# Optimization experiments

Measured on AMD Instinct MI355X. Metric: run time of the kernel, lower is better.

## Reference

```python
import jax, jax.numpy as jnp
import numpy as np

D_MODEL = 1024
N_HEADS = 16
HEAD_DIM = D_MODEL // N_HEADS


def setup_inputs() -> dict:
    key = jax.random.key(0)
    ks = jax.random.split(key, 5)
    B, S = 4, 2048
    scale = 1.0 / np.sqrt(D_MODEL)
    return {
        "x": jax.random.normal(ks[0], (B, S, D_MODEL), dtype=jnp.float32),
        "W_q": jax.random.normal(ks[1], (D_MODEL, D_MODEL), dtype=jnp.float32) * scale,
        "W_k": jax.random.normal(ks[2], (D_MODEL, D_MODEL), dtype=jnp.float32) * scale,
        "W_v": jax.random.normal(ks[3], (D_MODEL, D_MODEL), dtype=jnp.float32) * scale,
        "W_o": jax.random.normal(ks[4], (D_MODEL, D_MODEL), dtype=jnp.float32) * scale,
    }


def reference(x, W_q, W_k, W_v, W_o):
    B, S, _ = x.shape
    # nn.Linear(d,d,bias=False): y = x @ W.T ; W stored as (out,in)
    def proj(W):
        y = jnp.einsum('bsd,ed->bse', x, W)
        return y.reshape(B, S, N_HEADS, HEAD_DIM).transpose(0, 2, 1, 3)  # (B,H,S,Dh)
    q, k, v = proj(W_q), proj(W_k), proj(W_v)
    scores = jnp.einsum('bhqd,bhkd->bhqk', q, k) / np.sqrt(HEAD_DIM)
    causal = jnp.tril(jnp.ones((S, S), dtype=bool))  # (S,S)
    scores = jnp.where(causal[None, None], scores, -jnp.inf)
    attn = jax.nn.softmax(scores, axis=-1)
    heads = jnp.einsum('bhqk,bhkd->bhqd', attn, v)
    concat = heads.transpose(0, 2, 1, 3).reshape(B, S, D_MODEL)
    return jnp.einsum('bsd,ed->bse', concat, W_o)
```

## Files before the change

kernel.cpp:

```cpp
#include <hip/hip_runtime.h>
#include <hip/hip_bf16.h>

#define D_MODEL 1024
#define N_HEADS 16
#define HEAD_DIM 64
#define BATCH 4
#define SEQ 2048
#define M_ROWS (BATCH * SEQ)

typedef __attribute__((ext_vector_type(8))) __bf16 bf16x8;
typedef __attribute__((ext_vector_type(8))) short short8;
typedef __attribute__((ext_vector_type(4))) float f32x4;

static __device__ __forceinline__ unsigned short f2bf_rne(float f) {
  unsigned int u = __float_as_uint(f);
  u += 0x7FFFu + ((u >> 16) & 1u);
  return (unsigned short)(u >> 16);
}

static __device__ __forceinline__ void gl_lds16(const unsigned short* g, unsigned short* l) {
  __builtin_amdgcn_global_load_lds((const __attribute__((address_space(1))) unsigned int*)g,
                                   (__attribute__((address_space(3))) unsigned int*)l, 16, 0, 0);
}

__global__ __launch_bounds__(256) void cvt_all(const float* __restrict__ x,
                                               const float* __restrict__ wq,
                                               const float* __restrict__ wk,
                                               const float* __restrict__ wv,
                                               const float* __restrict__ wo,
                                               unsigned short* __restrict__ xb,
                                               unsigned short* __restrict__ wqb,
                                               unsigned short* __restrict__ wkb,
                                               unsigned short* __restrict__ wvb,
                                               unsigned short* __restrict__ wob) {
  const int bid = blockIdx.x;
  const float* src;
  unsigned short* dst;
  int i;
  if (bid < 8192) {
    src = x; dst = xb; i = bid * 256 + threadIdx.x;
  } else {
    int r = bid - 8192;
    int w = r >> 10;
    i = (r & 1023) * 256 + threadIdx.x;
    switch (w) {
      case 0: src = wq; dst = wqb; break;
      case 1: src = wk; dst = wkb; break;
      case 2: src = wv; dst = wvb; break;
      default: src = wo; dst = wob; break;
    }
  }
  float4 f = reinterpret_cast<const float4*>(src)[i];
  ushort4 o;
  o.x = f2bf_rne(f.x); o.y = f2bf_rne(f.y); o.z = f2bf_rne(f.z); o.w = f2bf_rne(f.w);
  reinterpret_cast<ushort4*>(dst)[i] = o;
}

__global__ __launch_bounds__(256) void qkv_gemm(const unsigned short* __restrict__ A,
                                                const unsigned short* __restrict__ Wq,
                                                const unsigned short* __restrict__ Wk,
                                                const unsigned short* __restrict__ Wv,
                                                unsigned short* __restrict__ Qo,
                                                unsigned short* __restrict__ Ko,
                                                unsigned short* __restrict__ Vo) {
  __shared__ __align__(16) unsigned short As[128 * 32];
  __shared__ __align__(16) unsigned short Bs[128 * 32];
  const int t = threadIdx.x;
  const int widx = blockIdx.x >> 3;
  const int bn = blockIdx.x & 7, bm = blockIdx.y;
  const unsigned short* Bw = (widx == 0) ? Wq : (widx == 1) ? Wk : Wv;
  unsigned short* Cp = (widx == 0) ? Qo : (widx == 1) ? Ko : Vo;
  const float oscale = (widx == 0) ? 0.125f : 1.0f;
  const int K = D_MODEL, N = D_MODEL;

  const int wave = t >> 6, lane = t & 63;
  const int wm = (wave >> 1) * 64, wn = (wave & 1) * 64;
  const int lr = lane & 15, quad = lane >> 4;

  f32x4 acc[4][4] = {};

  for (int k0 = 0; k0 < K; k0 += 32) {
    __syncthreads();
#pragma unroll
    for (int i = 0; i < 2; i++) {
      int g = wave * 128 + i * 64 + lane;
      int row = g >> 2, col8 = (g & 3) << 3;
      gl_lds16(A + (size_t)(bm * 128 + row) * K + k0 + col8, &As[g * 8]);
      gl_lds16(Bw + (size_t)(bn * 128 + row) * K + k0 + col8, &Bs[g * 8]);
    }
    __syncthreads();

    bf16x8 af[4], bfr[4];
#pragma unroll
    for (int mt = 0; mt < 4; mt++)
      af[mt] = __builtin_bit_cast(
          bf16x8, *reinterpret_cast<const short8*>(&As[(wm + mt * 16 + lr) * 32 + quad * 8]));
#pragma unroll
    for (int nt = 0; nt < 4; nt++)
      bfr[nt] = __builtin_bit_cast(
          bf16x8, *reinterpret_cast<const short8*>(&Bs[(wn + nt * 16 + lr) * 32 + quad * 8]));
#pragma unroll
    for (int mt = 0; mt < 4; mt++)
#pragma unroll
      for (int nt = 0; nt < 4; nt++)
        acc[mt][nt] = __builtin_amdgcn_mfma_f32_16x16x32_bf16(af[mt], bfr[nt], acc[mt][nt], 0, 0, 0);
  }

#pragma unroll
  for (int mt = 0; mt < 4; mt++) {
#pragma unroll
    for (int nt = 0; nt < 4; nt++) {
      int col = bn * 128 + wn + nt * 16 + lr;
#pragma unroll
      for (int r = 0; r < 4; r++) {
        int row = bm * 128 + wm + mt * 16 + quad * 4 + r;
        Cp[(size_t)row * N + col] = f2bf_rne(acc[mt][nt][r] * oscale);
      }
    }
  }
}

__global__ __launch_bounds__(256) void gemm_bt_f32(const unsigned short* __restrict__ A,
                                                   const unsigned short* __restrict__ Bw,
                                                   float* __restrict__ Cp,
                                                   int M, int N, int K) {
  __shared__ __align__(16) unsigned short As[128 * 32];
  __shared__ __align__(16) unsigned short Bs[128 * 32];
  const int t = threadIdx.x;
  const int bn = blockIdx.x, bm = blockIdx.y;
  const int wave = t >> 6, lane = t & 63;
  const int wm = (wave >> 1) * 64, wn = (wave & 1) * 64;
  const int lr = lane & 15, quad = lane >> 4;

  f32x4 acc[4][4] = {};

  for (int k0 = 0; k0 < K; k0 += 32) {
    __syncthreads();
#pragma unroll
    for (int i = 0; i < 2; i++) {
      int g = wave * 128 + i * 64 + lane;
      int row = g >> 2, col8 = (g & 3) << 3;
      gl_lds16(A + (size_t)(bm * 128 + row) * K + k0 + col8, &As[g * 8]);
      gl_lds16(Bw + (size_t)(bn * 128 + row) * K + k0 + col8, &Bs[g * 8]);
    }
    __syncthreads();

    bf16x8 af[4], bfr[4];
#pragma unroll
    for (int mt = 0; mt < 4; mt++)
      af[mt] = __builtin_bit_cast(
          bf16x8, *reinterpret_cast<const short8*>(&As[(wm + mt * 16 + lr) * 32 + quad * 8]));
#pragma unroll
    for (int nt = 0; nt < 4; nt++)
      bfr[nt] = __builtin_bit_cast(
          bf16x8, *reinterpret_cast<const short8*>(&Bs[(wn + nt * 16 + lr) * 32 + quad * 8]));
#pragma unroll
    for (int mt = 0; mt < 4; mt++)
#pragma unroll
      for (int nt = 0; nt < 4; nt++)
        acc[mt][nt] = __builtin_amdgcn_mfma_f32_16x16x32_bf16(af[mt], bfr[nt], acc[mt][nt], 0, 0, 0);
  }

#pragma unroll
  for (int mt = 0; mt < 4; mt++) {
#pragma unroll
    for (int nt = 0; nt < 4; nt++) {
      int col = bn * 128 + wn + nt * 16 + lr;
#pragma unroll
      for (int r = 0; r < 4; r++) {
        int row = bm * 128 + wm + mt * 16 + quad * 4 + r;
        Cp[(size_t)row * N + col] = acc[mt][nt][r];
      }
    }
  }
}

__global__ __launch_bounds__(256) void transpose_v(const unsigned short* __restrict__ V,
                                                   unsigned short* __restrict__ Vt) {
  __shared__ __align__(16) unsigned short tile[64][72];
  const int b = blockIdx.z, h = blockIdx.y, s0 = blockIdx.x * 64;
  const int t = threadIdx.x;
#pragma unroll
  for (int p = 0; p < 2; p++) {
    int c = p * 256 + t;
    int r = c >> 3, c8 = (c & 7) * 8;
    uint4 v = *reinterpret_cast<const uint4*>(V + (size_t)(b * SEQ + s0 + r) * D_MODEL + h * 64 + c8);
    *reinterpret_cast<uint4*>(&tile[r][c8]) = v;
  }
  __syncthreads();
#pragma unroll
  for (int p = 0; p < 2; p++) {
    int c = p * 256 + t;
    int d = c >> 3, s8 = (c & 7) * 8;
    unsigned short o[8];
#pragma unroll
    for (int j = 0; j < 8; j++) o[j] = tile[s8 + j][d];
    *reinterpret_cast<uint4*>(Vt + ((size_t)((b * N_HEADS + h) * HEAD_DIM + d)) * SEQ + s0 + s8) =
        *reinterpret_cast<const uint4*>(o);
  }
}

__global__ __launch_bounds__(256, 4) void attn_causal(const unsigned short* __restrict__ Q,
                                                      const unsigned short* __restrict__ Km,
                                                      const unsigned short* __restrict__ Vt,
                                                      unsigned short* __restrict__ O) {
  __shared__ __align__(16) unsigned short Ks[64 * 72];
  __shared__ __align__(16) unsigned short Vs[64 * 72];
  __shared__ __align__(16) unsigned short Ps[4][16 * 72];

  const int bid = blockIdx.x;
  const int p = bid & 15;
  const int h = (bid >> 4) & 15;
  const int b = bid >> 8;

  const int t = threadIdx.x;
  const int wave = t >> 6, lane = t & 63;
  const int lr = lane & 15, quad = lane >> 4;

  const size_t base = (size_t)b * SEQ * D_MODEL + h * HEAD_DIM;
  const unsigned short* Qb = Q + base;
  const unsigned short* Kb = Km + base;
  const unsigned short* Vb = Vt + (size_t)(b * N_HEADS + h) * HEAD_DIM * SEQ;
  unsigned short* pw = &Ps[wave][0];

  const int sr = t >> 3, sc = (t & 7) << 3;

  for (int ph = 0; ph < 2; ph++) {
    const int qt = ph ? (31 - p) : p;
    const int m0 = qt * 64 + wave * 16;
    const int ntiles = qt + 1;

    bf16x8 qf[2];
#pragma unroll
    for (int kk = 0; kk < 2; kk++)
      qf[kk] = __builtin_bit_cast(
          bf16x8,
          *reinterpret_cast<const short8*>(Qb + (size_t)(m0 + lr) * D_MODEL + kk * 32 + quad * 8));

    f32x4 o_acc[4] = {};
    float lsum[4] = {};

    uint4 ra = *reinterpret_cast<const uint4*>(Kb + (size_t)sr * D_MODEL + sc);
    uint4 rb = *reinterpret_cast<const uint4*>(Kb + (size_t)(sr + 32) * D_MODEL + sc);
    uint4 rc = *reinterpret_cast<const uint4*>(Vb + (size_t)sr * SEQ + sc);
    uint4 rd = *reinterpret_cast<const uint4*>(Vb + (size_t)(sr + 32) * SEQ + sc);

    for (int kt = 0; kt < ntiles; kt++) {
      const int kv0 = kt * 64;
      __syncthreads();
      *reinterpret_cast<uint4*>(&Ks[sr * 72 + sc]) = ra;
      *reinterpret_cast<uint4*>(&Ks[(sr + 32) * 72 + sc]) = rb;
      *reinterpret_cast<uint4*>(&Vs[sr * 72 + sc]) = rc;
      *reinterpret_cast<uint4*>(&Vs[(sr + 32) * 72 + sc]) = rd;
      __syncthreads();
      if (kt + 1 < ntiles) {
        const int kv1 = kv0 + 64;
        ra = *reinterpret_cast<const uint4*>(Kb + (size_t)(kv1 + sr) * D_MODEL + sc);
        rb = *reinterpret_cast<const uint4*>(Kb + (size_t)(kv1 + sr + 32) * D_MODEL + sc);
        rc = *reinterpret_cast<const uint4*>(Vb + (size_t)sr * SEQ + kv1 + sc);
        rd = *reinterpret_cast<const uint4*>(Vb + (size_t)(sr + 32) * SEQ + kv1 + sc);
      }

      f32x4 sAcc[4] = {};
#pragma unroll
      for (int kk = 0; kk < 2; kk++) {
        bf16x8 kf[4];
#pragma unroll
        for (int j = 0; j < 4; j++)
          kf[j] = __builtin_bit_cast(
              bf16x8, *reinterpret_cast<const short8*>(&Ks[(j * 16 + lr) * 72 + kk * 32 + quad * 8]));
#pragma unroll
        for (int j = 0; j < 4; j++)
          sAcc[j] = __builtin_amdgcn_mfma_f32_16x16x32_bf16(qf[kk], kf[j], sAcc[j], 0, 0, 0);
      }

      asm volatile("s_waitcnt lgkmcnt(0)" ::: "memory");
      const bool needmask = (kt == qt) || (kt == qt - 0);
#pragma unroll
      for (int r = 0; r < 4; r++) {
        const int qpos = m0 + quad * 4 + r;
        float e[4];
#pragma unroll
        for (int j = 0; j < 4; j++) e[j] = __expf(sAcc[j][r]);
        if (kt == ntiles - 1) {
#pragma unroll
          for (int j = 0; j < 4; j++)
            if (kv0 + j * 16 + lr > qpos) e[j] = 0.f;
        }
        lsum[r] += (e[0] + e[1]) + (e[2] + e[3]);
        unsigned short* pr = &pw[(quad * 4 + r) * 72];
#pragma unroll
        for (int j = 0; j < 4; j++) pr[j * 16 + lr] = f2bf_rne(e[j]);
      }
      asm volatile("s_waitcnt lgkmcnt(0)" ::: "memory");

#pragma unroll
      for (int kk = 0; kk < 2; kk++) {
        bf16x8 pf = __builtin_bit_cast(
            bf16x8, *reinterpret_cast<const short8*>(&pw[lr * 72 + kk * 32 + quad * 8]));
#pragma unroll
        for (int c = 0; c < 4; c++) {
          bf16x8 vv = __builtin_bit_cast(
              bf16x8, *reinterpret_cast<const short8*>(&Vs[(c * 16 + lr) * 72 + kk * 32 + quad * 8]));
          o_acc[c] = __builtin_amdgcn_mfma_f32_16x16x32_bf16(pf, vv, o_acc[c], 0, 0, 0);
        }
      }
    }

#pragma unroll
    for (int r = 0; r < 4; r++) {
      float l = lsum[r];
#pragma unroll
      for (int off = 1; off < 16; off <<= 1) l += __shfl_xor(l, off, 64);
      const float inv = 1.f / l;
      const int qpos = m0 + quad * 4 + r;
#pragma unroll
      for (int c = 0; c < 4; c++)
        O[base + (size_t)qpos * D_MODEL + c * 16 + lr] = f2bf_rne(o_acc[c][r] * inv);
    }
  }
}

extern "C" void kernel_launch(void* const* d_in, const int* in_sizes, int n_in,
                              void* d_out, int out_size, void* d_ws, size_t ws_size,
                              hipStream_t stream) {
  const float* x  = (const float*)d_in[0];
  const float* Wq = (const float*)d_in[1];
  const float* Wk = (const float*)d_in[2];
  const float* Wv = (const float*)d_in[3];
  const float* Wo = (const float*)d_in[4];
  float* out = (float*)d_out;

  char* ws = (char*)d_ws;
  const size_t SZ_X = (size_t)M_ROWS * D_MODEL * 2;
  const size_t SZ_W = (size_t)D_MODEL * D_MODEL * 2;
  unsigned short* xb  = (unsigned short*)(ws);
  unsigned short* wqb = (unsigned short*)(ws + SZ_X);
  unsigned short* wkb = (unsigned short*)(ws + SZ_X + 1 * SZ_W);
  unsigned short* wvb = (unsigned short*)(ws + SZ_X + 2 * SZ_W);
  unsigned short* wob = (unsigned short*)(ws + SZ_X + 3 * SZ_W);
  unsigned short* Qb  = (unsigned short*)(ws + 1 * SZ_X + 4 * SZ_W);
  unsigned short* Kb  = (unsigned short*)(ws + 2 * SZ_X + 4 * SZ_W);
  unsigned short* Vbf = (unsigned short*)(ws + 3 * SZ_X + 4 * SZ_W);
  unsigned short* Vt  = (unsigned short*)(ws + 4 * SZ_X + 4 * SZ_W);
  unsigned short* Ob  = xb;

  cvt_all<<<12288, 256, 0, stream>>>(x, Wq, Wk, Wv, Wo, xb, wqb, wkb, wvb, wob);

  qkv_gemm<<<dim3(24, 64), 256, 0, stream>>>(xb, wqb, wkb, wvb, Qb, Kb, Vbf);

  transpose_v<<<dim3(SEQ / 64, N_HEADS, BATCH), 256, 0, stream>>>(Vbf, Vt);

  attn_causal<<<1024, 256, 0, stream>>>(Qb, Kb, Vt, Ob);

  gemm_bt_f32<<<dim3(8, 64), 256, 0, stream>>>(Ob, wob, out, M_ROWS, D_MODEL, D_MODEL);
}
```

Baseline: 284.1 us.

## Fuse V transpose into QKV GEMM epilogue and use exp2 softmax

The V projection's epilogue now writes a head-transposed V directly through shared memory, so the separate transpose kernel and its intermediate buffer are gone. The Q output scale folds in log2(e), which lets the attention kernel use the native exp2 instruction instead of exp. The attention block-to-work mapping is reordered so query-tile pairs are the slow index, which changes how work is scheduled across CUs and how it interacts with the cache. The extra barriers in the GEMM epilogue add a little cost to V blocks.

```diff
diff --git a/kernel.cpp b/kernel.cpp
--- a/kernel.cpp
+++ b/kernel.cpp
@@ -17,6 +17,12 @@
   u += 0x7FFFu + ((u >> 16) & 1u);
   return (unsigned short)(u >> 16);
 }
+
+#if __has_builtin(__builtin_amdgcn_exp2f)
+#define EXP2F(x) __builtin_amdgcn_exp2f(x)
+#else
+#define EXP2F(x) exp2f(x)
+#endif
 
 static __device__ __forceinline__ void gl_lds16(const unsigned short* g, unsigned short* l) {
   __builtin_amdgcn_global_load_lds((const __attribute__((address_space(1))) unsigned int*)g,
@@ -62,15 +68,16 @@
                                                 const unsigned short* __restrict__ Wv,
                                                 unsigned short* __restrict__ Qo,
                                                 unsigned short* __restrict__ Ko,
-                                                unsigned short* __restrict__ Vo) {
-  __shared__ __align__(16) unsigned short As[128 * 32];
-  __shared__ __align__(16) unsigned short Bs[128 * 32];
+                                                unsigned short* __restrict__ Vt) {
+  __shared__ __align__(16) unsigned short smem[64 * 136];
+  unsigned short* As = smem;
+  unsigned short* Bs = smem + 4096;
+
   const int t = threadIdx.x;
   const int widx = blockIdx.x >> 3;
   const int bn = blockIdx.x & 7, bm = blockIdx.y;
   const unsigned short* Bw = (widx == 0) ? Wq : (widx == 1) ? Wk : Wv;
-  unsigned short* Cp = (widx == 0) ? Qo : (widx == 1) ? Ko : Vo;
-  const float oscale = (widx == 0) ? 0.125f : 1.0f;
+  const float oscale = (widx == 0) ? 0.18033688f : 1.0f;
   const int K = D_MODEL, N = D_MODEL;
 
   const int wave = t >> 6, lane = t & 63;
@@ -106,15 +113,49 @@
         acc[mt][nt] = __builtin_amdgcn_mfma_f32_16x16x32_bf16(af[mt], bfr[nt], acc[mt][nt], 0, 0, 0);
   }
 
-#pragma unroll
-  for (int mt = 0; mt < 4; mt++) {
-#pragma unroll
-    for (int nt = 0; nt < 4; nt++) {
-      int col = bn * 128 + wn + nt * 16 + lr;
-#pragma unroll
-      for (int r = 0; r < 4; r++) {
-        int row = bm * 128 + wm + mt * 16 + quad * 4 + r;
-        Cp[(size_t)row * N + col] = f2bf_rne(acc[mt][nt][r] * oscale);
+  if (widx < 2) {
+    unsigned short* Cp = (widx == 0) ? Qo : Ko;
+#pragma unroll
+    for (int mt = 0; mt < 4; mt++) {
+#pragma unroll
+      for (int nt = 0; nt < 4; nt++) {
+        int col = bn * 128 + wn + nt * 16 + lr;
+#pragma unroll
+        for (int r = 0; r < 4; r++) {
+          int row = bm * 128 + wm + mt * 16 + quad * 4 + r;
+          Cp[(size_t)row * N + col] = f2bf_rne(acc[mt][nt][r] * oscale);
+        }
+      }
+    }
+  } else {
+    const int b = bm >> 4;
+    const int s0 = (bm & 15) * 128;
+#pragma unroll
+    for (int half = 0; half < 2; half++) {
+      __syncthreads();
+      if ((wave & 1) == half) {
+#pragma unroll
+        for (int nt = 0; nt < 4; nt++) {
+#pragma unroll
+          for (int mt = 0; mt < 4; mt++) {
+#pragma unroll
+            for (int r = 0; r < 4; r++) {
+              int cl = nt * 16 + lr;
+              int rl = wm + mt * 16 + quad * 4 + r;
+              smem[cl * 136 + rl] = f2bf_rne(acc[mt][nt][r]);
+            }
+          }
+        }
+      }
+      __syncthreads();
+      const int h2 = bn * 2 + half;
+      const size_t rowbase = ((size_t)(b * N_HEADS + h2)) * HEAD_DIM;
+#pragma unroll
+      for (int i = 0; i < 4; i++) {
+        int c = i * 256 + t;
+        int d = c >> 4, s8 = (c & 15) * 8;
+        uint4 v = *reinterpret_cast<const uint4*>(&smem[d * 136 + s8]);
+        *reinterpret_cast<uint4*>(Vt + (rowbase + d) * SEQ + s0 + s8) = v;
       }
     }
   }
@@ -175,31 +216,6 @@
   }
 }
 
-__global__ __launch_bounds__(256) void transpose_v(const unsigned short* __restrict__ V,
-                                                   unsigned short* __restrict__ Vt) {
-  __shared__ __align__(16) unsigned short tile[64][72];
-  const int b = blockIdx.z, h = blockIdx.y, s0 = blockIdx.x * 64;
-  const int t = threadIdx.x;
-#pragma unroll
-  for (int p = 0; p < 2; p++) {
-    int c = p * 256 + t;
-    int r = c >> 3, c8 = (c & 7) * 8;
-    uint4 v = *reinterpret_cast<const uint4*>(V + (size_t)(b * SEQ + s0 + r) * D_MODEL + h * 64 + c8);
-    *reinterpret_cast<uint4*>(&tile[r][c8]) = v;
-  }
-  __syncthreads();
-#pragma unroll
-  for (int p = 0; p < 2; p++) {
-    int c = p * 256 + t;
-    int d = c >> 3, s8 = (c & 7) * 8;
-    unsigned short o[8];
-#pragma unroll
-    for (int j = 0; j < 8; j++) o[j] = tile[s8 + j][d];
-    *reinterpret_cast<uint4*>(Vt + ((size_t)((b * N_HEADS + h) * HEAD_DIM + d)) * SEQ + s0 + s8) =
-        *reinterpret_cast<const uint4*>(o);
-  }
-}
-
 __global__ __launch_bounds__(256, 4) void attn_causal(const unsigned short* __restrict__ Q,
                                                       const unsigned short* __restrict__ Km,
                                                       const unsigned short* __restrict__ Vt,
@@ -209,9 +225,10 @@
   __shared__ __align__(16) unsigned short Ps[4][16 * 72];
 
   const int bid = blockIdx.x;
-  const int p = bid & 15;
-  const int h = (bid >> 4) & 15;
-  const int b = bid >> 8;
+  const int p = bid >> 6;
+  const int bh = bid & 63;
+  const int h = bh & 15;
+  const int b = bh >> 4;
 
   const int t = threadIdx.x;
   const int wave = t >> 6, lane = t & 63;
@@ -275,13 +292,12 @@
       }
 
       asm volatile("s_waitcnt lgkmcnt(0)" ::: "memory");
-      const bool needmask = (kt == qt) || (kt == qt - 0);
 #pragma unroll
       for (int r = 0; r < 4; r++) {
         const int qpos = m0 + quad * 4 + r;
         float e[4];
 #pragma unroll
-        for (int j = 0; j < 4; j++) e[j] = __expf(sAcc[j][r]);
+        for (int j = 0; j < 4; j++) e[j] = EXP2F(sAcc[j][r]);
         if (kt == ntiles - 1) {
 #pragma unroll
           for (int j = 0; j < 4; j++)
@@ -341,15 +357,12 @@
   unsigned short* wob = (unsigned short*)(ws + SZ_X + 3 * SZ_W);
   unsigned short* Qb  = (unsigned short*)(ws + 1 * SZ_X + 4 * SZ_W);
   unsigned short* Kb  = (unsigned short*)(ws + 2 * SZ_X + 4 * SZ_W);
-  unsigned short* Vbf = (unsigned short*)(ws + 3 * SZ_X + 4 * SZ_W);
-  unsigned short* Vt  = (unsigned short*)(ws + 4 * SZ_X + 4 * SZ_W);
+  unsigned short* Vt  = (unsigned short*)(ws + 3 * SZ_X + 4 * SZ_W);
   unsigned short* Ob  = xb;
 
   cvt_all<<<12288, 256, 0, stream>>>(x, Wq, Wk, Wv, Wo, xb, wqb, wkb, wvb, wob);
 
-  qkv_gemm<<<dim3(24, 64), 256, 0, stream>>>(xb, wqb, wkb, wvb, Qb, Kb, Vbf);
-
-  transpose_v<<<dim3(SEQ / 64, N_HEADS, BATCH), 256, 0, stream>>>(Vbf, Vt);
+  qkv_gemm<<<dim3(24, 64), 256, 0, stream>>>(xb, wqb, wkb, wvb, Qb, Kb, Vt);
 
   attn_causal<<<1024, 256, 0, stream>>>(Qb, Kb, Vt, Ob);
 
```

After: 311.9 us. +9.8%, slower.
